# Optimization experiments

Hardware: AMD Instinct MI355X
Metric: run time of the kernel (lower is better)

## Reference

```python
import jax, jax.numpy as jnp
import numpy as np

N = 100000      # num nodes
M = 25000       # num hyperedges
E = 600000      # num incidences (node, hyperedge) pairs
D_IN, D_HID, D_OUT = 128, 128, 128


def setup_inputs() -> dict:
    key = jax.random.key(0)
    ks = jax.random.split(key, 9)
    s_in = 1.0 / np.sqrt(D_IN)
    s_hid = 1.0 / np.sqrt(D_HID)
    return {
        "x": jax.random.normal(ks[0], (N, D_IN), dtype=jnp.float32),
        "W1": jax.random.normal(ks[1], (D_IN, D_HID), dtype=jnp.float32) * s_in,
        "b1": jnp.zeros((D_HID,), dtype=jnp.float32),
        "W2": jax.random.normal(ks[2], (D_HID, D_HID), dtype=jnp.float32) * s_hid,
        "b2": jnp.zeros((D_HID,), dtype=jnp.float32),
        "W3": jax.random.normal(ks[3], (D_HID, D_OUT), dtype=jnp.float32) * s_hid,
        "b3": jnp.zeros((D_OUT,), dtype=jnp.float32),
        "node_idx": jax.random.randint(ks[4], (E,), 0, N, dtype=jnp.int32),
        "hedge_idx": jax.random.randint(ks[5], (E,), 0, M, dtype=jnp.int32),
        "num_hyperedges": M,
    }


def _hypergraph_conv(x, W, b, node_idx, hedge_idx, num_hyperedges):
    """PyG HypergraphConv (use_attention=False, hyperedge_weight=1):
    out = D^-1 H B^-1 H^T (x @ W) + b
    """
    n = x.shape[0]
    x = x @ W                                   # [N, F_out]
    ones = jnp.ones(node_idx.shape[0], dtype=x.dtype)
    deg_n = jax.ops.segment_sum(ones, node_idx, num_segments=n)              # D
    deg_e = jax.ops.segment_sum(ones, hedge_idx, num_segments=num_hyperedges)  # B
    d_inv = jnp.where(deg_n > 0, 1.0 / deg_n, 0.0)
    b_inv = jnp.where(deg_e > 0, 1.0 / deg_e, 0.0)
    # node -> hyperedge: m_e = B^-1 sum_{i in e} x_i
    m = jax.ops.segment_sum(x[node_idx], hedge_idx, num_segments=num_hyperedges)
    m = m * b_inv[:, None]
    # hyperedge -> node: out_i = D^-1 sum_{e ni i} m_e
    out = jax.ops.segment_sum(m[hedge_idx], node_idx, num_segments=n)
    out = out * d_inv[:, None]
    return out + b


def reference(x, W1, b1, W2, b2, W3, b3, node_idx, hedge_idx, num_hyperedges):
    # dropout is identity in eval mode (training=False)
    x = jax.nn.elu(_hypergraph_conv(x, W1, b1, node_idx, hedge_idx, num_hyperedges))
    x = jax.nn.elu(_hypergraph_conv(x, W2, b2, node_idx, hedge_idx, num_hyperedges))
    x = jax.nn.elu(_hypergraph_conv(x, W3, b3, node_idx, hedge_idx, num_hyperedges))
    return x
```

## Files before the change

kernel.cpp:

```cpp
#include <hip/hip_runtime.h>

#define NN 100000
#define MM 25000
#define EE 600000
#define TT (MM + NN)

#define CVT_BLOCKS 12500
#define NB 782
#define TILE_E 4096
#define GA ((EE + TILE_E - 1) / TILE_E)

typedef __attribute__((ext_vector_type(8))) short short8;
typedef __attribute__((ext_vector_type(4))) float floatx4;

__device__ __forceinline__ float bl(unsigned int u){ return __uint_as_float(u << 16); }
__device__ __forceinline__ float bh(unsigned int u){ return __uint_as_float(u & 0xffff0000u); }
__device__ __forceinline__ unsigned int packbf2(float a, float b){
    unsigned int ua = __float_as_uint(a), ub = __float_as_uint(b);
    ua = (ua + 0x7fffu + ((ua >> 16) & 1u)) >> 16;
    ub = (ub + 0x7fffu + ((ub >> 16) & 1u)) & 0xffff0000u;
    return ua | ub;
}
__device__ __forceinline__ unsigned short f2bf(float f){
    unsigned int u = __float_as_uint(f);
    return (unsigned short)((u + 0x7fffu + ((u >> 16) & 1u)) >> 16);
}
__device__ __forceinline__ void acc8(float* a, uint4 v){
    a[0] += bl(v.x); a[1] += bh(v.x);
    a[2] += bl(v.y); a[3] += bh(v.y);
    a[4] += bl(v.z); a[5] += bh(v.z);
    a[6] += bl(v.w); a[7] += bh(v.w);
}

__global__ void k_setup(const float* __restrict__ x, unsigned int* __restrict__ xb,
                        const float* __restrict__ W1, const float* __restrict__ W2,
                        const float* __restrict__ W3, unsigned short* __restrict__ WT) {
    int b = blockIdx.x;
    if (b < CVT_BLOCKS) {
        int t = b * 256 + threadIdx.x;
        float4 v = ((const float4*)x)[t];
        uint2 o; o.x = packbf2(v.x, v.y); o.y = packbf2(v.z, v.w);
        ((uint2*)xb)[t] = o;
    } else {
        int l = b - CVT_BLOCKS;
        const float* W = l == 0 ? W1 : (l == 1 ? W2 : W3);
        unsigned short* T = WT + l * 16384;
        for (int i = threadIdx.x; i < 16384; i += 256) {
            int k = i >> 7, c = i & 127;
            T[c * 128 + k] = f2bf(W[k * 128 + c]);
        }
    }
}

__global__ __launch_bounds__(256) void k_histA(const int* __restrict__ nidx, const int* __restrict__ hidx,
                                               int* __restrict__ counts) {
    __shared__ int h[NB];
    int t = threadIdx.x;
    for (int i = t; i < NB; i += 256) h[i] = 0;
    __syncthreads();
    int base = blockIdx.x * TILE_E;
    #pragma unroll
    for (int k = 0; k < 16; k++) {
        int e = base + k * 256 + t;
        if (e < EE) {
            atomicAdd(&h[hidx[e] >> 6], 1);
            atomicAdd(&h[391 + (nidx[e] >> 8)], 1);
        }
    }
    __syncthreads();
    for (int i = t; i < NB; i += 256) counts[blockIdx.x * NB + i] = h[i];
}

__global__ __launch_bounds__(1024) void k_scanA(int* __restrict__ counts, int* __restrict__ bbase) {
    __shared__ int tot[1024];
    int t = threadIdx.x;
    int run = 0;
    if (t < NB) {
        for (int b = 0; b < GA; b++) {
            int c = counts[b * NB + t];
            counts[b * NB + t] = run;
            run += c;
        }
    }
    tot[t] = (t < NB) ? run : 0;
    __syncthreads();
    for (int o = 1; o < 1024; o <<= 1) {
        int v = (t >= o) ? tot[t - o] : 0;
        __syncthreads();
        tot[t] += v;
        __syncthreads();
    }
    if (t < NB) bbase[t] = tot[t] - run;
    if (t == NB - 1) bbase[NB] = tot[t];
}

__global__ __launch_bounds__(256) void k_scatA(const int* __restrict__ nidx, const int* __restrict__ hidx,
                                               const int* __restrict__ counts, const int* __restrict__ bbase,
                                               unsigned int* __restrict__ items) {
    __shared__ int cur[NB];
    int t = threadIdx.x;
    for (int i = t; i < NB; i += 256) cur[i] = bbase[i] + counts[blockIdx.x * NB + i];
    __syncthreads();
    int base = blockIdx.x * TILE_E;
    #pragma unroll
    for (int k = 0; k < 16; k++) {
        int e = base + k * 256 + t;
        if (e < EE) {
            int hh = hidx[e], nn = nidx[e];
            int p1 = atomicAdd(&cur[hh >> 6], 1);
            items[p1] = ((unsigned)(hh & 63) << 17) | (unsigned)nn;
            int p2 = atomicAdd(&cur[391 + (nn >> 8)], 1);
            items[p2] = ((unsigned)(nn & 255) << 15) | (unsigned)hh;
        }
    }
}

__global__ __launch_bounds__(256) void k_passB(unsigned int* __restrict__ items,
                                               const int* __restrict__ bbase,
                                               int* __restrict__ ptr, float* __restrict__ inv) {
    __shared__ unsigned int led[3072];
    __shared__ unsigned int grp[3072];
    __shared__ int bins[256], cur[256], tmp[256];
    int b = blockIdx.x, t = threadIdx.x;
    int base = bbase[b], cnt = bbase[b + 1] - base;
    bool he = b < 391;
    int nbins = he ? 64 : 256;
    int keybase = he ? b * 64 : MM + (b - 391) * 256;
    int shift = he ? 17 : 15;
    unsigned int mask = he ? 0x1FFFFu : 0x7FFFu;
    int keylim = he ? MM : TT;

    for (int i = t; i < cnt; i += 256) led[i] = items[base + i];
    if (t < 256) bins[t] = 0;
    __syncthreads();
    for (int i = t; i < cnt; i += 256) atomicAdd(&bins[led[i] >> shift], 1);
    __syncthreads();
    int v = (t < nbins) ? bins[t] : 0;
    tmp[t] = v;
    __syncthreads();
    for (int o = 1; o < 256; o <<= 1) {
        int u = (t >= o) ? tmp[t - o] : 0;
        __syncthreads();
        tmp[t] += u;
        __syncthreads();
    }
    int excl = tmp[t] - v;
    if (t < nbins) {
        int g = keybase + t;
        if (g < keylim) {
            ptr[g] = base + excl;
            inv[g] = v ? 1.f / (float)v : 0.f;
        }
        cur[t] = excl;
    }
    __syncthreads();
    for (int i = t; i < cnt; i += 256) {
        unsigned int it = led[i];
        int p = atomicAdd(&cur[it >> shift], 1);
        grp[p] = it & mask;
    }
    __syncthreads();
    for (int i = t; i < cnt; i += 256) items[base + i] = grp[i];
    if (b == NB - 1 && t == 0) ptr[TT] = 2 * EE;
}

__device__ __forceinline__ void gather_row(const unsigned int* __restrict__ X,
                                           const int* __restrict__ adj,
                                           int beg, int end, int ql, float* a) {
    for (int j = beg; j < end; j += 4) {
        int c = end - j;
        int n0 = adj[j];
        int n1 = (c > 1) ? adj[j + 1] : 0;
        int n2 = (c > 2) ? adj[j + 2] : 0;
        int n3 = (c > 3) ? adj[j + 3] : 0;
        uint4 v0 = *((const uint4*)(X + (unsigned)n0 * 64u) + ql);
        uint4 z = make_uint4(0u, 0u, 0u, 0u);
        uint4 v1 = z, v2 = z, v3 = z;
        if (c > 1) v1 = *((const uint4*)(X + (unsigned)n1 * 64u) + ql);
        if (c > 2) v2 = *((const uint4*)(X + (unsigned)n2 * 64u) + ql);
        if (c > 3) v3 = *((const uint4*)(X + (unsigned)n3 * 64u) + ql);
        acc8(a, v0); acc8(a, v1); acc8(a, v2); acc8(a, v3);
    }
}

__global__ __launch_bounds__(256) void k_gather_he(const unsigned int* __restrict__ X,
        const int* __restrict__ ptr, const int* __restrict__ adj,
        const float* __restrict__ b_inv, unsigned int* __restrict__ s) {
    int gw = (blockIdx.x * 256 + threadIdx.x) >> 6;
    int lane = threadIdx.x & 63, quad = lane >> 4, ql = lane & 15;
    int r = gw * 4 + quad;
    if (r >= MM) return;
    int beg = ptr[r], end = ptr[r + 1];
    float a[8] = {0.f,0.f,0.f,0.f,0.f,0.f,0.f,0.f};
    gather_row(X, adj, beg, end, ql, a);
    float sc = b_inv[r];
    uint4 o;
    o.x = packbf2(a[0] * sc, a[1] * sc);
    o.y = packbf2(a[2] * sc, a[3] * sc);
    o.z = packbf2(a[4] * sc, a[5] * sc);
    o.w = packbf2(a[6] * sc, a[7] * sc);
    ((uint4*)(s + (unsigned)r * 64u))[ql] = o;
}

template<bool F32OUT>
__global__ __launch_bounds__(256) void k_gather_nd(const unsigned int* __restrict__ X,
        const int* __restrict__ ptr, const int* __restrict__ adj,
        const float* __restrict__ d_inv, const float* __restrict__ bias, void* __restrict__ out) {
    int gw = (blockIdx.x * 256 + threadIdx.x) >> 6;
    int lane = threadIdx.x & 63, quad = lane >> 4, ql = lane & 15;
    int r = gw * 4 + quad;
    if (r >= NN) return;
    int beg = ptr[r], end = ptr[r + 1];
    float a[8] = {0.f,0.f,0.f,0.f,0.f,0.f,0.f,0.f};
    gather_row(X, adj, beg, end, ql, a);
    float sc = d_inv[r];
    const float4* b4 = (const float4*)bias;
    float4 bA = b4[ql * 2], bB = b4[ql * 2 + 1];
    float f[8];
    f[0] = a[0] * sc + bA.x; f[1] = a[1] * sc + bA.y;
    f[2] = a[2] * sc + bA.z; f[3] = a[3] * sc + bA.w;
    f[4] = a[4] * sc + bB.x; f[5] = a[5] * sc + bB.y;
    f[6] = a[6] * sc + bB.z; f[7] = a[7] * sc + bB.w;
    #pragma unroll
    for (int i = 0; i < 8; i++) f[i] = f[i] > 0.f ? f[i] : __expf(f[i]) - 1.f;
    if (F32OUT) {
        float* o = (float*)out + (unsigned)r * 128u;
        ((float4*)o)[ql * 2]     = make_float4(f[0], f[1], f[2], f[3]);
        ((float4*)o)[ql * 2 + 1] = make_float4(f[4], f[5], f[6], f[7]);
    } else {
        uint4 o4;
        o4.x = packbf2(f[0], f[1]); o4.y = packbf2(f[2], f[3]);
        o4.z = packbf2(f[4], f[5]); o4.w = packbf2(f[6], f[7]);
        ((uint4*)((unsigned int*)out + (unsigned)r * 64u))[ql] = o4;
    }
}

__global__ __launch_bounds__(256) void k_gemm(const unsigned short* __restrict__ A,
                                              const unsigned short* __restrict__ WT,
                                              unsigned short* __restrict__ C) {
    int lane = threadIdx.x & 63;
    int wv = threadIdx.x >> 6;
    int r0 = blockIdx.x * 64 + wv * 16;
    int mm = lane & 15;
    int quad = lane >> 4;
    floatx4 acc[8];
    #pragma unroll
    for (int c = 0; c < 8; c++) acc[c] = (floatx4){0.f, 0.f, 0.f, 0.f};
    int arow = r0 + mm; if (arow >= MM) arow = MM - 1;
    #pragma unroll
    for (int q = 0; q < 4; q++) {
        short8 af = *reinterpret_cast<const short8*>(A + arow * 128 + q * 32 + quad * 8);
        #pragma unroll
        for (int c = 0; c < 8; c++) {
            short8 bf = *reinterpret_cast<const short8*>(WT + (c * 16 + mm) * 128 + q * 32 + quad * 8);
            acc[c] = __builtin_amdgcn_mfma_f32_16x16x32_bf16(af, bf, acc[c], 0, 0, 0);
        }
    }
    #pragma unroll
    for (int c = 0; c < 8; c++) {
        #pragma unroll
        for (int r = 0; r < 4; r++) {
            int row = r0 + quad * 4 + r;
            if (row < MM) C[row * 128 + c * 16 + mm] = f2bf(acc[c][r]);
        }
    }
}

extern "C" void kernel_launch(void* const* d_in, const int* in_sizes, int n_in,
                              void* d_out, int out_size, void* d_ws, size_t ws_size,
                              hipStream_t stream) {
    const float* x  = (const float*)d_in[0];
    const float* W1 = (const float*)d_in[1];
    const float* b1 = (const float*)d_in[2];
    const float* W2 = (const float*)d_in[3];
    const float* b2 = (const float*)d_in[4];
    const float* W3 = (const float*)d_in[5];
    const float* b3 = (const float*)d_in[6];
    const int* nidx = (const int*)d_in[7];
    const int* hidx = (const int*)d_in[8];

    char* ws = (char*)d_ws;
    size_t o = 0;
    auto alloc = [&](size_t b) -> char* { char* p = ws + o; o = (o + b + 255) & ~(size_t)255; return p; };
    int*   ptr    = (int*)alloc((TT + 1) * 4);
    float* invq   = (float*)alloc(TT * 4);
    int*   counts = (int*)alloc((size_t)GA * NB * 4);
    int*   bbase  = (int*)alloc((NB + 1) * 4);
    int*   adj    = (int*)alloc((size_t)2 * EE * 4);
    unsigned short* WT   = (unsigned short*)alloc(3 * 128 * 128 * 2);
    unsigned short* sbuf = (unsigned short*)alloc((size_t)MM * 128 * 2);
    unsigned short* mbuf = (unsigned short*)alloc((size_t)MM * 128 * 2);

    unsigned int* xb   = (unsigned int*)d_out;
    unsigned int* bufA = (unsigned int*)d_out;
    unsigned int* bufB = (unsigned int*)d_out + (size_t)NN * 64;

    k_setup<<<CVT_BLOCKS + 3, 256, 0, stream>>>(x, xb, W1, W2, W3, WT);
    k_histA<<<GA, 256, 0, stream>>>(nidx, hidx, counts);
    k_scanA<<<1, 1024, 0, stream>>>(counts, bbase);
    k_scatA<<<GA, 256, 0, stream>>>(nidx, hidx, counts, bbase, (unsigned int*)adj);
    k_passB<<<NB, 256, 0, stream>>>((unsigned int*)adj, bbase, ptr, invq);

    const float* b_inv = invq;
    const float* d_inv = invq + MM;
    const int* nptr = ptr + MM;
    const int* nadj = adj;
    const int grid_he = (MM / 4 * 64 + 255) / 256;
    const int grid_nd = (NN / 4 * 64 + 255) / 256;
    const int grid_gm = (MM + 63) / 64;

    k_gather_he<<<grid_he, 256, 0, stream>>>(xb, ptr, adj, b_inv, (unsigned int*)sbuf);
    k_gemm<<<grid_gm, 256, 0, stream>>>(sbuf, WT, mbuf);
    k_gather_nd<false><<<grid_nd, 256, 0, stream>>>((const unsigned int*)mbuf, nptr, nadj, d_inv, b1, (void*)bufA);
    k_gather_he<<<grid_he, 256, 0, stream>>>(bufA, ptr, adj, b_inv, (unsigned int*)sbuf);
    k_gemm<<<grid_gm, 256, 0, stream>>>(sbuf, WT + 16384, mbuf);
    k_gather_nd<false><<<grid_nd, 256, 0, stream>>>((const unsigned int*)mbuf, nptr, nadj, d_inv, b2, (void*)bufB);
    k_gather_he<<<grid_he, 256, 0, stream>>>(bufB, ptr, adj, b_inv, (unsigned int*)sbuf);
    k_gemm<<<grid_gm, 256, 0, stream>>>(sbuf, WT + 32768, mbuf);
    k_gather_nd<true ><<<grid_nd, 256, 0, stream>>>((const unsigned int*)mbuf, nptr, nadj, d_inv, b3, d_out);
}
```

Measured before the change: 364.9 us.

## Fuse hyperedge gather with GEMM and bin incidences into fixed-capacity buckets

Drops the histogram, scan and scatter pipeline. Incidences now go into fixed-capacity buckets (CAP=2048 per bin), claimed through global atomic cursors that k_setup initialises, which removes two kernel launches and the per-tile count buffer. The hyperedge gather is fused with the bf16 MFMA GEMM in one kernel through a shared-memory tile, so the intermediate sbuf round trip and three launches go away. The gather loop is also unrolled to 8 neighbours, and an int2 (offset, degree) pointer replaces the CSR end lookups. The cost is a risk of bucket overflow on skewed inputs, run-to-run nondeterministic item order, and a node-gather grid that launches 4x more blocks than it needs, most of which exit early.

```diff
diff --git a/kernel.cpp b/kernel.cpp
--- a/kernel.cpp
+++ b/kernel.cpp
@@ -7,6 +7,7 @@
 
 #define CVT_BLOCKS 12500
 #define NB 782
+#define CAP 2048
 #define TILE_E 4096
 #define GA ((EE + TILE_E - 1) / TILE_E)
 
@@ -34,14 +35,15 @@
 
 __global__ void k_setup(const float* __restrict__ x, unsigned int* __restrict__ xb,
                         const float* __restrict__ W1, const float* __restrict__ W2,
-                        const float* __restrict__ W3, unsigned short* __restrict__ WT) {
+                        const float* __restrict__ W3, unsigned short* __restrict__ WT,
+                        int* __restrict__ gcur) {
     int b = blockIdx.x;
     if (b < CVT_BLOCKS) {
         int t = b * 256 + threadIdx.x;
         float4 v = ((const float4*)x)[t];
         uint2 o; o.x = packbf2(v.x, v.y); o.y = packbf2(v.z, v.w);
         ((uint2*)xb)[t] = o;
-    } else {
+    } else if (b < CVT_BLOCKS + 3) {
         int l = b - CVT_BLOCKS;
         const float* W = l == 0 ? W1 : (l == 1 ? W2 : W3);
         unsigned short* T = WT + l * 16384;
@@ -49,12 +51,15 @@
             int k = i >> 7, c = i & 127;
             T[c * 128 + k] = f2bf(W[k * 128 + c]);
         }
-    }
-}
-
-__global__ __launch_bounds__(256) void k_histA(const int* __restrict__ nidx, const int* __restrict__ hidx,
-                                               int* __restrict__ counts) {
+    } else {
+        for (int i = threadIdx.x; i < NB; i += 256) gcur[i] = i * CAP;
+    }
+}
+
+__global__ __launch_bounds__(256) void k_binA(const int* __restrict__ nidx, const int* __restrict__ hidx,
+                                              int* __restrict__ gcur, unsigned int* __restrict__ items) {
     __shared__ int h[NB];
+    __shared__ int cur[NB];
     int t = threadIdx.x;
     for (int i = t; i < NB; i += 256) h[i] = 0;
     __syncthreads();
@@ -68,40 +73,11 @@
         }
     }
     __syncthreads();
-    for (int i = t; i < NB; i += 256) counts[blockIdx.x * NB + i] = h[i];
-}
-
-__global__ __launch_bounds__(1024) void k_scanA(int* __restrict__ counts, int* __restrict__ bbase) {
-    __shared__ int tot[1024];
-    int t = threadIdx.x;
-    int run = 0;
-    if (t < NB) {
-        for (int b = 0; b < GA; b++) {
-            int c = counts[b * NB + t];
-            counts[b * NB + t] = run;
-            run += c;
-        }
-    }
-    tot[t] = (t < NB) ? run : 0;
-    __syncthreads();
-    for (int o = 1; o < 1024; o <<= 1) {
-        int v = (t >= o) ? tot[t - o] : 0;
-        __syncthreads();
-        tot[t] += v;
-        __syncthreads();
-    }
-    if (t < NB) bbase[t] = tot[t] - run;
-    if (t == NB - 1) bbase[NB] = tot[t];
-}
-
-__global__ __launch_bounds__(256) void k_scatA(const int* __restrict__ nidx, const int* __restrict__ hidx,
-                                               const int* __restrict__ counts, const int* __restrict__ bbase,
-                                               unsigned int* __restrict__ items) {
-    __shared__ int cur[NB];
-    int t = threadIdx.x;
-    for (int i = t; i < NB; i += 256) cur[i] = bbase[i] + counts[blockIdx.x * NB + i];
-    __syncthreads();
-    int base = blockIdx.x * TILE_E;
+    for (int i = t; i < NB; i += 256) {
+        int c = h[i];
+        cur[i] = c ? atomicAdd(&gcur[i], c) : 0;
+    }
+    __syncthreads();
     #pragma unroll
     for (int k = 0; k < 16; k++) {
         int e = base + k * 256 + t;
@@ -116,13 +92,13 @@
 }
 
 __global__ __launch_bounds__(256) void k_passB(unsigned int* __restrict__ items,
-                                               const int* __restrict__ bbase,
-                                               int* __restrict__ ptr, float* __restrict__ inv) {
-    __shared__ unsigned int led[3072];
-    __shared__ unsigned int grp[3072];
+                                               const int* __restrict__ gcur,
+                                               int2* __restrict__ ptr2, float* __restrict__ inv) {
+    __shared__ unsigned int led[CAP];
+    __shared__ unsigned int grp[CAP];
     __shared__ int bins[256], cur[256], tmp[256];
     int b = blockIdx.x, t = threadIdx.x;
-    int base = bbase[b], cnt = bbase[b + 1] - base;
+    int base = b * CAP, cnt = gcur[b] - base;
     bool he = b < 391;
     int nbins = he ? 64 : 256;
     int keybase = he ? b * 64 : MM + (b - 391) * 256;
@@ -131,7 +107,7 @@
     int keylim = he ? MM : TT;
 
     for (int i = t; i < cnt; i += 256) led[i] = items[base + i];
-    if (t < 256) bins[t] = 0;
+    bins[t] = 0;
     __syncthreads();
     for (int i = t; i < cnt; i += 256) atomicAdd(&bins[led[i] >> shift], 1);
     __syncthreads();
@@ -148,7 +124,7 @@
     if (t < nbins) {
         int g = keybase + t;
         if (g < keylim) {
-            ptr[g] = base + excl;
+            ptr2[g] = make_int2(base + excl, v);
             inv[g] = v ? 1.f / (float)v : 0.f;
         }
         cur[t] = excl;
@@ -161,58 +137,86 @@
     }
     __syncthreads();
     for (int i = t; i < cnt; i += 256) items[base + i] = grp[i];
-    if (b == NB - 1 && t == 0) ptr[TT] = 2 * EE;
-}
-
-__device__ __forceinline__ void gather_row(const unsigned int* __restrict__ X,
-                                           const int* __restrict__ adj,
-                                           int beg, int end, int ql, float* a) {
-    for (int j = beg; j < end; j += 4) {
+}
+
+__device__ __forceinline__ void gather_row8(const unsigned int* __restrict__ X,
+                                            const unsigned int* __restrict__ adj,
+                                            int beg, int deg, int ql, float* a) {
+    int end = beg + deg;
+    for (int j = beg; j < end; j += 8) {
         int c = end - j;
-        int n0 = adj[j];
-        int n1 = (c > 1) ? adj[j + 1] : 0;
-        int n2 = (c > 2) ? adj[j + 2] : 0;
-        int n3 = (c > 3) ? adj[j + 3] : 0;
-        uint4 v0 = *((const uint4*)(X + (unsigned)n0 * 64u) + ql);
+        int n[8];
+        #pragma unroll
+        for (int i = 0; i < 8; i++) n[i] = (i < c) ? (int)adj[j + i] : 0;
         uint4 z = make_uint4(0u, 0u, 0u, 0u);
-        uint4 v1 = z, v2 = z, v3 = z;
-        if (c > 1) v1 = *((const uint4*)(X + (unsigned)n1 * 64u) + ql);
-        if (c > 2) v2 = *((const uint4*)(X + (unsigned)n2 * 64u) + ql);
-        if (c > 3) v3 = *((const uint4*)(X + (unsigned)n3 * 64u) + ql);
-        acc8(a, v0); acc8(a, v1); acc8(a, v2); acc8(a, v3);
-    }
-}
-
-__global__ __launch_bounds__(256) void k_gather_he(const unsigned int* __restrict__ X,
-        const int* __restrict__ ptr, const int* __restrict__ adj,
-        const float* __restrict__ b_inv, unsigned int* __restrict__ s) {
-    int gw = (blockIdx.x * 256 + threadIdx.x) >> 6;
-    int lane = threadIdx.x & 63, quad = lane >> 4, ql = lane & 15;
-    int r = gw * 4 + quad;
-    if (r >= MM) return;
-    int beg = ptr[r], end = ptr[r + 1];
+        uint4 v[8];
+        #pragma unroll
+        for (int i = 0; i < 8; i++) {
+            v[i] = z;
+            if (i < c) v[i] = *((const uint4*)(X + (unsigned)n[i] * 64u) + ql);
+        }
+        #pragma unroll
+        for (int i = 0; i < 8; i++) acc8(a, v[i]);
+    }
+}
+
+__global__ __launch_bounds__(256) void k_hegemm(const unsigned int* __restrict__ X,
+        const int2* __restrict__ ptr2, const unsigned int* __restrict__ adj,
+        const float* __restrict__ b_inv, const unsigned short* __restrict__ WT,
+        unsigned short* __restrict__ C) {
+    __shared__ unsigned int tile[16 * 68];
+    int t = threadIdx.x;
+    int qidx = t >> 4, ql = t & 15;
+    int r0 = blockIdx.x * 16;
+    int r = r0 + qidx;
     float a[8] = {0.f,0.f,0.f,0.f,0.f,0.f,0.f,0.f};
-    gather_row(X, adj, beg, end, ql, a);
-    float sc = b_inv[r];
+    float sc = 0.f;
+    if (r < MM) {
+        int2 pe = ptr2[r];
+        gather_row8(X, adj, pe.x, pe.y, ql, a);
+        sc = b_inv[r];
+    }
     uint4 o;
     o.x = packbf2(a[0] * sc, a[1] * sc);
     o.y = packbf2(a[2] * sc, a[3] * sc);
     o.z = packbf2(a[4] * sc, a[5] * sc);
     o.w = packbf2(a[6] * sc, a[7] * sc);
-    ((uint4*)(s + (unsigned)r * 64u))[ql] = o;
+    *((uint4*)(tile + qidx * 68 + ql * 4)) = o;
+    __syncthreads();
+
+    int wv = t >> 6, lane = t & 63;
+    int mm = lane & 15, quad = lane >> 4;
+    floatx4 acc0 = (floatx4){0.f,0.f,0.f,0.f}, acc1 = acc0;
+    int c0 = wv * 2;
+    #pragma unroll
+    for (int q = 0; q < 4; q++) {
+        short8 af = *reinterpret_cast<const short8*>((const short*)(tile + mm * 68) + q * 32 + quad * 8);
+        short8 b0 = *reinterpret_cast<const short8*>(WT + (c0 * 16 + mm) * 128 + q * 32 + quad * 8);
+        short8 b1 = *reinterpret_cast<const short8*>(WT + ((c0 + 1) * 16 + mm) * 128 + q * 32 + quad * 8);
+        acc0 = __builtin_amdgcn_mfma_f32_16x16x32_bf16(af, b0, acc0, 0, 0, 0);
+        acc1 = __builtin_amdgcn_mfma_f32_16x16x32_bf16(af, b1, acc1, 0, 0, 0);
+    }
+    #pragma unroll
+    for (int rg = 0; rg < 4; rg++) {
+        int rr = r0 + quad * 4 + rg;
+        if (rr < MM) {
+            C[rr * 128 + c0 * 16 + mm]       = f2bf(acc0[rg]);
+            C[rr * 128 + (c0 + 1) * 16 + mm] = f2bf(acc1[rg]);
+        }
+    }
 }
 
 template<bool F32OUT>
 __global__ __launch_bounds__(256) void k_gather_nd(const unsigned int* __restrict__ X,
-        const int* __restrict__ ptr, const int* __restrict__ adj,
+        const int2* __restrict__ ptr2, const unsigned int* __restrict__ adj,
         const float* __restrict__ d_inv, const float* __restrict__ bias, void* __restrict__ out) {
     int gw = (blockIdx.x * 256 + threadIdx.x) >> 6;
     int lane = threadIdx.x & 63, quad = lane >> 4, ql = lane & 15;
     int r = gw * 4 + quad;
     if (r >= NN) return;
-    int beg = ptr[r], end = ptr[r + 1];
+    int2 pe = ptr2[r];
     float a[8] = {0.f,0.f,0.f,0.f,0.f,0.f,0.f,0.f};
-    gather_row(X, adj, beg, end, ql, a);
+    gather_row8(X, adj, pe.x, pe.y, ql, a);
     float sc = d_inv[r];
     const float4* b4 = (const float4*)bias;
     float4 bA = b4[ql * 2], bB = b4[ql * 2 + 1];
@@ -232,37 +236,6 @@
         o4.x = packbf2(f[0], f[1]); o4.y = packbf2(f[2], f[3]);
         o4.z = packbf2(f[4], f[5]); o4.w = packbf2(f[6], f[7]);
         ((uint4*)((unsigned int*)out + (unsigned)r * 64u))[ql] = o4;
-    }
-}
-
-__global__ __launch_bounds__(256) void k_gemm(const unsigned short* __restrict__ A,
-                                              const unsigned short* __restrict__ WT,
-                                              unsigned short* __restrict__ C) {
-    int lane = threadIdx.x & 63;
-    int wv = threadIdx.x >> 6;
-    int r0 = blockIdx.x * 64 + wv * 16;
-    int mm = lane & 15;
-    int quad = lane >> 4;
-    floatx4 acc[8];
-    #pragma unroll
-    for (int c = 0; c < 8; c++) acc[c] = (floatx4){0.f, 0.f, 0.f, 0.f};
-    int arow = r0 + mm; if (arow >= MM) arow = MM - 1;
-    #pragma unroll
-    for (int q = 0; q < 4; q++) {
-        short8 af = *reinterpret_cast<const short8*>(A + arow * 128 + q * 32 + quad * 8);
-        #pragma unroll
-        for (int c = 0; c < 8; c++) {
-            short8 bf = *reinterpret_cast<const short8*>(WT + (c * 16 + mm) * 128 + q * 32 + quad * 8);
-            acc[c] = __builtin_amdgcn_mfma_f32_16x16x32_bf16(af, bf, acc[c], 0, 0, 0);
-        }
-    }
-    #pragma unroll
-    for (int c = 0; c < 8; c++) {
-        #pragma unroll
-        for (int r = 0; r < 4; r++) {
-            int row = r0 + quad * 4 + r;
-            if (row < MM) C[row * 128 + c * 16 + mm] = f2bf(acc[c][r]);
-        }
     }
 }
 
@@ -282,40 +255,32 @@
     char* ws = (char*)d_ws;
     size_t o = 0;
     auto alloc = [&](size_t b) -> char* { char* p = ws + o; o = (o + b + 255) & ~(size_t)255; return p; };
-    int*   ptr    = (int*)alloc((TT + 1) * 4);
-    float* invq   = (float*)alloc(TT * 4);
-    int*   counts = (int*)alloc((size_t)GA * NB * 4);
-    int*   bbase  = (int*)alloc((NB + 1) * 4);
-    int*   adj    = (int*)alloc((size_t)2 * EE * 4);
+    int2*  ptr2  = (int2*)alloc((size_t)TT * 8);
+    float* invq  = (float*)alloc(TT * 4);
+    int*   gcur  = (int*)alloc(NB * 4);
+    unsigned int* items = (unsigned int*)alloc((size_t)NB * CAP * 4);
     unsigned short* WT   = (unsigned short*)alloc(3 * 128 * 128 * 2);
-    unsigned short* sbuf = (unsigned short*)alloc((size_t)MM * 128 * 2);
     unsigned short* mbuf = (unsigned short*)alloc((size_t)MM * 128 * 2);
 
     unsigned int* xb   = (unsigned int*)d_out;
     unsigned int* bufA = (unsigned int*)d_out;
     unsigned int* bufB = (unsigned int*)d_out + (size_t)NN * 64;
 
-    k_setup<<<CVT_BLOCKS + 3, 256, 0, stream>>>(x, xb, W1, W2, W3, WT);
-    k_histA<<<GA, 256, 0, stream>>>(nidx, hidx, counts);
-    k_scanA<<<1, 1024, 0, stream>>>(counts, bbase);
-    k_scatA<<<GA, 256, 0, stream>>>(nidx, hidx, counts, bbase, (unsigned int*)adj);
-    k_passB<<<NB, 256, 0, stream>>>((unsigned int*)adj, bbase, ptr, invq);
+    k_setup<<<CVT_BLOCKS + 4, 256, 0, stream>>>(x, xb, W1, W2, W3, WT, gcur);
+    k_binA<<<GA, 256, 0, stream>>>(nidx, hidx, gcur, items);
+    k_passB<<<NB, 256, 0, stream>>>(items, gcur, ptr2, invq);
 
     const float* b_inv = invq;
     const float* d_inv = invq + MM;
-    const int* nptr = ptr + MM;
-    const int* nadj = adj;
-    const int grid_he = (MM / 4 * 64 + 255) / 256;
-    const int grid_nd = (NN / 4 * 64 + 255) / 256;
-    const int grid_gm = (MM + 63) / 64;
-
-    k_gather_he<<<grid_he, 256, 0, stream>>>(xb, ptr, adj, b_inv, (unsigned int*)sbuf);
-    k_gemm<<<grid_gm, 256, 0, stream>>>(sbuf, WT, mbuf);
-    k_gather_nd<false><<<grid_nd, 256, 0, stream>>>((const unsigned int*)mbuf, nptr, nadj, d_inv, b1, (void*)bufA);
-    k_gather_he<<<grid_he, 256, 0, stream>>>(bufA, ptr, adj, b_inv, (unsigned int*)sbuf);
-    k_gemm<<<grid_gm, 256, 0, stream>>>(sbuf, WT + 16384, mbuf);
-    k_gather_nd<false><<<grid_nd, 256, 0, stream>>>((const unsigned int*)mbuf, nptr, nadj, d_inv, b2, (void*)bufB);
-    k_gather_he<<<grid_he, 256, 0, stream>>>(bufB, ptr, adj, b_inv, (unsigned int*)sbuf);
-    k_gemm<<<grid_gm, 256, 0, stream>>>(sbuf, WT + 32768, mbuf);
-    k_gather_nd<true ><<<grid_nd, 256, 0, stream>>>((const unsigned int*)mbuf, nptr, nadj, d_inv, b3, d_out);
-}
+    const int2* nptr2 = ptr2 + MM;
+    const int grid_hg = (MM + 15) / 16;
+    const int grid_nd = NN * 64 / 256;
+    const unsigned int* adj = items;
+
+    k_hegemm<<<grid_hg, 256, 0, stream>>>(xb, ptr2, adj, b_inv, WT, mbuf);
+    k_gather_nd<false><<<grid_nd, 256, 0, stream>>>((const unsigned int*)mbuf, nptr2, adj, d_inv, b1, (void*)bufA);
+    k_hegemm<<<grid_hg, 256, 0, stream>>>(bufA, ptr2, adj, b_inv, WT + 16384, mbuf);
+    k_gather_nd<false><<<grid_nd, 256, 0, stream>>>((const unsigned int*)mbuf, nptr2, adj, d_inv, b2, (void*)bufB);
+    k_hegemm<<<grid_hg, 256, 0, stream>>>(bufB, ptr2, adj, b_inv, WT + 32768, mbuf);
+    k_gather_nd<true ><<<grid_nd, 256, 0, stream>>>((const unsigned int*)mbuf, nptr2, adj, d_inv, b3, d_out);
+}
```

New measurement: 362.2 us. About the same (-0.7%).
